# Performance work log

Measured on AMD Instinct MI355X. Metric: run time of the kernel, lower is better.

## Reference

```python
import jax, jax.numpy as jnp
import numpy as np

EPS_BN = 0.001

def setup_inputs() -> dict:
    key = jax.random.key(0)
    ks = jax.random.split(key, 11)
    B, C, H, W = 32, 512, 64, 64
    Hc = 128
    return {
        'x':  jax.random.normal(ks[0], (B, C, H, W), dtype=jnp.float32),
        'w1': jax.random.normal(ks[1], (Hc, C), dtype=jnp.float32) * (1.0 / np.sqrt(C)),
        'g1': jax.random.uniform(ks[2], (Hc,), dtype=jnp.float32, minval=0.5, maxval=1.5),
        'b1': jax.random.normal(ks[3], (Hc,), dtype=jnp.float32) * 0.1,
        'm1': jax.random.normal(ks[4], (Hc,), dtype=jnp.float32) * 0.1,
        'v1': jax.random.uniform(ks[5], (Hc,), dtype=jnp.float32, minval=0.5, maxval=1.5),
        'w2': jax.random.normal(ks[6], (C, Hc), dtype=jnp.float32) * (1.0 / np.sqrt(Hc)),
        'g2': jax.random.uniform(ks[7], (C,), dtype=jnp.float32, minval=0.5, maxval=1.5),
        'b2': jax.random.normal(ks[8], (C,), dtype=jnp.float32) * 0.1,
        'm2': jax.random.normal(ks[9], (C,), dtype=jnp.float32) * 0.1,
        'v2': jax.random.uniform(ks[10], (C,), dtype=jnp.float32, minval=0.5, maxval=1.5),
    }

def reference(x, w1, g1, b1, m1, v1, w2, g2, b2, m2, v2):
    # squeeze: global average pool -> [B, C]
    s = jnp.mean(x, axis=(2, 3))
    # excitation: 1x1 conv (C->Hc, no bias), eval-mode BN, ReLU, 1x1 conv (Hc->C, no bias)
    h = jnp.einsum('bc,hc->bh', s, w1)
    h = (h - m1) * (g1 * jax.lax.rsqrt(v1 + EPS_BN)) + b1
    h = jax.nn.relu(h)
    e = jnp.einsum('bh,ch->bc', h, w2)  # scale_activation = Identity
    # broadcast scale + final eval-mode BN over channels
    y = x * e[:, :, None, None]
    scale2 = (g2 * jax.lax.rsqrt(v2 + EPS_BN))[None, :, None, None]
    shift2 = (b2 - m2 * g2 * jax.lax.rsqrt(v2 + EPS_BN))[None, :, None, None]
    return y * scale2 + shift2
```

## Files before the change

### kernel.cpp

```cpp
#include <hip/hip_runtime.h>
#include <hip/hip_bf16.h>
#include <stdint.h>

#define B_   32
#define C_   512
#define HW_  4096
#define HC_  128
#define EPS_ 1e-3f

typedef uint32_t u32x4 __attribute__((ext_vector_type(4)));
typedef float    f32x4 __attribute__((ext_vector_type(4)));

__device__ __forceinline__ float bf_lo(uint32_t u) { return __uint_as_float(u << 16); }
__device__ __forceinline__ float bf_hi(uint32_t u) { return __uint_as_float(u & 0xffff0000u); }

__device__ __forceinline__ uint32_t packbf2(float lo, float hi) {
    union { uint32_t u; __hip_bfloat162 h; } cv;
    cv.h.x = __float2bfloat16(lo);
    cv.h.y = __float2bfloat16(hi);
    return cv.u;
}

__device__ __forceinline__ float ld_scalar(const void* p, int i, int isbf) {
    if (isbf) return __bfloat162float(((const __hip_bfloat16*)p)[i]);
    return ((const float*)p)[i];
}

template <int NT>
__device__ __forceinline__ int detect_isbf(const uint32_t* __restrict__ v2w,
                                           int t, int* s_flag) {
    if (t == 0) *s_flag = 1;
    __syncthreads();
    bool ok = true;
    #pragma unroll
    for (int i = t; i < 256; i += NT) {
        const uint32_t w = v2w[i];
        const float lo = bf_lo(w), hi = bf_hi(w);
        ok = ok && (lo >= 0.4f) && (lo <= 1.6f) && (hi >= 0.4f) && (hi <= 1.6f);
    }
    if (!ok) *s_flag = 0;
    __syncthreads();
    return *s_flag;
}

__global__ __launch_bounds__(256) void se_pool(const void* __restrict__ x,
                                               float* __restrict__ s,
                                               const uint32_t* __restrict__ v2w) {
    __shared__ int s_flag;
    __shared__ float part[4];
    const int t  = threadIdx.x;
    const int isbf = detect_isbf<256>(v2w, t, &s_flag);
    const int bc = blockIdx.x;
    float sum = 0.f;
    if (isbf) {
        const u32x4* p = reinterpret_cast<const u32x4*>(x) + (size_t)bc * (HW_ / 8);
        #pragma unroll
        for (int i = t; i < HW_ / 8; i += 256) {
            u32x4 v = p[i];
            sum += bf_lo(v.x) + bf_hi(v.x) + bf_lo(v.y) + bf_hi(v.y)
                 + bf_lo(v.z) + bf_hi(v.z) + bf_lo(v.w) + bf_hi(v.w);
        }
    } else {
        const f32x4* p = reinterpret_cast<const f32x4*>(x) + (size_t)bc * (HW_ / 4);
        #pragma unroll
        for (int i = t; i < HW_ / 4; i += 256) {
            f32x4 v = p[i];
            sum += v.x + v.y + v.z + v.w;
        }
    }
    #pragma unroll
    for (int off = 32; off > 0; off >>= 1)
        sum += __shfl_down(sum, off, 64);
    if ((t & 63) == 0) part[t >> 6] = sum;
    __syncthreads();
    if (t == 0) {
        float tot = part[0] + part[1] + part[2] + part[3];
        s[bc] = tot * (1.0f / (float)HW_);
    }
}

__global__ __launch_bounds__(128) void se_excite(
    const float* __restrict__ s,
    const void* __restrict__ w1, const void* __restrict__ g1,
    const void* __restrict__ b1, const void* __restrict__ m1,
    const void* __restrict__ v1, const void* __restrict__ w2,
    const void* __restrict__ g2, const void* __restrict__ b2,
    const void* __restrict__ m2, const void* __restrict__ v2,
    float* __restrict__ A, float* __restrict__ S2) {
    __shared__ int s_flag;
    __shared__ float s_sh[C_];
    __shared__ float h_sh[HC_];
    const int b = blockIdx.x, t = threadIdx.x;
    const int isbf = detect_isbf<128>((const uint32_t*)v2, t, &s_flag);
    for (int i = t; i < C_; i += HC_) s_sh[i] = s[b * C_ + i];
    __syncthreads();

    float acc = 0.f;
    if (isbf) {
        const u32x4* w1r = reinterpret_cast<const u32x4*>(w1) + (size_t)t * (C_ / 8);
        #pragma unroll 8
        for (int i = 0; i < C_ / 8; ++i) {
            u32x4 v = w1r[i];
            const int c = i * 8;
            acc += s_sh[c + 0] * bf_lo(v.x) + s_sh[c + 1] * bf_hi(v.x)
                 + s_sh[c + 2] * bf_lo(v.y) + s_sh[c + 3] * bf_hi(v.y)
                 + s_sh[c + 4] * bf_lo(v.z) + s_sh[c + 5] * bf_hi(v.z)
                 + s_sh[c + 6] * bf_lo(v.w) + s_sh[c + 7] * bf_hi(v.w);
        }
    } else {
        const f32x4* w1r = reinterpret_cast<const f32x4*>(w1) + (size_t)t * (C_ / 4);
        #pragma unroll 8
        for (int i = 0; i < C_ / 4; ++i) {
            f32x4 v = w1r[i];
            const int c = i * 4;
            acc += s_sh[c + 0] * v.x + s_sh[c + 1] * v.y
                 + s_sh[c + 2] * v.z + s_sh[c + 3] * v.w;
        }
    }
    const float sc1 = ld_scalar(g1, t, isbf) * rsqrtf(ld_scalar(v1, t, isbf) + EPS_);
    const float hv  = (acc - ld_scalar(m1, t, isbf)) * sc1 + ld_scalar(b1, t, isbf);
    h_sh[t] = fmaxf(hv, 0.f);
    __syncthreads();

    #pragma unroll
    for (int k = 0; k < C_ / HC_; ++k) {
        const int c = t + HC_ * k;
        float e = 0.f;
        if (isbf) {
            const u32x4* w2r = reinterpret_cast<const u32x4*>(w2) + (size_t)c * (HC_ / 8);
            #pragma unroll
            for (int i = 0; i < HC_ / 8; ++i) {
                u32x4 v = w2r[i];
                const int j = i * 8;
                e += h_sh[j + 0] * bf_lo(v.x) + h_sh[j + 1] * bf_hi(v.x)
                   + h_sh[j + 2] * bf_lo(v.y) + h_sh[j + 3] * bf_hi(v.y)
                   + h_sh[j + 4] * bf_lo(v.z) + h_sh[j + 5] * bf_hi(v.z)
                   + h_sh[j + 6] * bf_lo(v.w) + h_sh[j + 7] * bf_hi(v.w);
            }
        } else {
            const f32x4* w2r = reinterpret_cast<const f32x4*>(w2) + (size_t)c * (HC_ / 4);
            #pragma unroll
            for (int i = 0; i < HC_ / 4; ++i) {
                f32x4 v = w2r[i];
                const int j = i * 4;
                e += h_sh[j + 0] * v.x + h_sh[j + 1] * v.y
                   + h_sh[j + 2] * v.z + h_sh[j + 3] * v.w;
            }
        }
        const float sc2 = ld_scalar(g2, c, isbf) * rsqrtf(ld_scalar(v2, c, isbf) + EPS_);
        A[b * C_ + c] = e * sc2;
        if (b == 0) S2[c] = ld_scalar(b2, c, isbf) - ld_scalar(m2, c, isbf) * sc2;
    }
}

__global__ __launch_bounds__(256) void se_apply(const void* __restrict__ x,
                                                const float* __restrict__ A,
                                                const float* __restrict__ S2,
                                                void* __restrict__ y,
                                                const uint32_t* __restrict__ v2w) {
    __shared__ int s_flag;
    const int t  = threadIdx.x;
    const int isbf = detect_isbf<256>(v2w, t, &s_flag);
    const int bc = (B_ * C_ - 1) - (int)blockIdx.x;
    const float a  = A[bc];
    const float sh = S2[bc & (C_ - 1)];
    if (isbf) {
        const u32x4* px = reinterpret_cast<const u32x4*>(x) + (size_t)bc * (HW_ / 8);
        u32x4*       py = reinterpret_cast<u32x4*>(y)       + (size_t)bc * (HW_ / 8);
        #pragma unroll
        for (int i = t; i < HW_ / 8; i += 256) {
            u32x4 v = px[i];
            u32x4 r;
            r.x = packbf2(fmaf(bf_lo(v.x), a, sh), fmaf(bf_hi(v.x), a, sh));
            r.y = packbf2(fmaf(bf_lo(v.y), a, sh), fmaf(bf_hi(v.y), a, sh));
            r.z = packbf2(fmaf(bf_lo(v.z), a, sh), fmaf(bf_hi(v.z), a, sh));
            r.w = packbf2(fmaf(bf_lo(v.w), a, sh), fmaf(bf_hi(v.w), a, sh));
            __builtin_nontemporal_store(r, py + i);
        }
    } else {
        const f32x4* px = reinterpret_cast<const f32x4*>(x) + (size_t)bc * (HW_ / 4);
        f32x4*       py = reinterpret_cast<f32x4*>(y)       + (size_t)bc * (HW_ / 4);
        #pragma unroll
        for (int i = t; i < HW_ / 4; i += 256) {
            f32x4 v = px[i];
            f32x4 r;
            r.x = fmaf(v.x, a, sh);
            r.y = fmaf(v.y, a, sh);
            r.z = fmaf(v.z, a, sh);
            r.w = fmaf(v.w, a, sh);
            __builtin_nontemporal_store(r, py + i);
        }
    }
}

extern "C" void kernel_launch(void* const* d_in, const int* in_sizes, int n_in,
                              void* d_out, int out_size, void* d_ws, size_t ws_size,
                              hipStream_t stream) {
    const void* x  = d_in[0];
    const void* w1 = d_in[1];
    const void* g1 = d_in[2];
    const void* b1 = d_in[3];
    const void* m1 = d_in[4];
    const void* v1 = d_in[5];
    const void* w2 = d_in[6];
    const void* g2 = d_in[7];
    const void* b2 = d_in[8];
    const void* m2 = d_in[9];
    const void* v2 = d_in[10];

    float* ws = (float*)d_ws;
    float* s  = ws;
    float* A  = ws + B_ * C_;
    float* S2 = ws + 2 * B_ * C_;

    se_pool<<<B_ * C_, 256, 0, stream>>>(x, s, (const uint32_t*)v2);
    se_excite<<<B_, HC_, 0, stream>>>(s, w1, g1, b1, m1, v1, w2, g2, b2, m2, v2,
                                      A, S2);
    se_apply<<<B_ * C_, 256, 0, stream>>>(x, A, S2, d_out, (const uint32_t*)v2);
}
```

Measured before the change: 523.6 us.

## Fuse pooling and excitation via last-block-per-batch atomic counter

Merges the pooling and excitation kernels into one. Each block pools one (b,c) channel, then increments a per-batch atomic counter, and the last block to finish for a batch runs the two small matvecs. This drops one kernel launch and its serialization bubble, but adds a memset launch, threadfences and an atomic per block. The dtype-detection loop is also simplified to a single load per thread.

```diff
diff --git a/kernel.cpp b/kernel.cpp
--- a/kernel.cpp
+++ b/kernel.cpp
@@ -26,108 +26,110 @@
     return ((const float*)p)[i];
 }
 
-template <int NT>
 __device__ __forceinline__ int detect_isbf(const uint32_t* __restrict__ v2w,
                                            int t, int* s_flag) {
     if (t == 0) *s_flag = 1;
     __syncthreads();
-    bool ok = true;
-    #pragma unroll
-    for (int i = t; i < 256; i += NT) {
-        const uint32_t w = v2w[i];
-        const float lo = bf_lo(w), hi = bf_hi(w);
-        ok = ok && (lo >= 0.4f) && (lo <= 1.6f) && (hi >= 0.4f) && (hi <= 1.6f);
-    }
+    const uint32_t w = v2w[t];
+    const float lo = bf_lo(w), hi = bf_hi(w);
+    const bool ok = (lo >= 0.4f) && (lo <= 1.6f) && (hi >= 0.4f) && (hi <= 1.6f);
     if (!ok) *s_flag = 0;
     __syncthreads();
     return *s_flag;
 }
 
-__global__ __launch_bounds__(256) void se_pool(const void* __restrict__ x,
-                                               float* __restrict__ s,
-                                               const uint32_t* __restrict__ v2w) {
-    __shared__ int s_flag;
-    __shared__ float part[4];
-    const int t  = threadIdx.x;
-    const int isbf = detect_isbf<256>(v2w, t, &s_flag);
-    const int bc = blockIdx.x;
-    float sum = 0.f;
-    if (isbf) {
-        const u32x4* p = reinterpret_cast<const u32x4*>(x) + (size_t)bc * (HW_ / 8);
-        #pragma unroll
-        for (int i = t; i < HW_ / 8; i += 256) {
-            u32x4 v = p[i];
-            sum += bf_lo(v.x) + bf_hi(v.x) + bf_lo(v.y) + bf_hi(v.y)
-                 + bf_lo(v.z) + bf_hi(v.z) + bf_lo(v.w) + bf_hi(v.w);
-        }
-    } else {
-        const f32x4* p = reinterpret_cast<const f32x4*>(x) + (size_t)bc * (HW_ / 4);
-        #pragma unroll
-        for (int i = t; i < HW_ / 4; i += 256) {
-            f32x4 v = p[i];
-            sum += v.x + v.y + v.z + v.w;
-        }
-    }
-    #pragma unroll
-    for (int off = 32; off > 0; off >>= 1)
-        sum += __shfl_down(sum, off, 64);
-    if ((t & 63) == 0) part[t >> 6] = sum;
-    __syncthreads();
-    if (t == 0) {
-        float tot = part[0] + part[1] + part[2] + part[3];
-        s[bc] = tot * (1.0f / (float)HW_);
-    }
-}
-
-__global__ __launch_bounds__(128) void se_excite(
-    const float* __restrict__ s,
+__global__ __launch_bounds__(256) void se_pool_excite(
+    const void* __restrict__ x,
     const void* __restrict__ w1, const void* __restrict__ g1,
     const void* __restrict__ b1, const void* __restrict__ m1,
     const void* __restrict__ v1, const void* __restrict__ w2,
     const void* __restrict__ g2, const void* __restrict__ b2,
     const void* __restrict__ m2, const void* __restrict__ v2,
-    float* __restrict__ A, float* __restrict__ S2) {
-    __shared__ int s_flag;
+    float* __restrict__ s, float* __restrict__ A, float* __restrict__ S2,
+    int* __restrict__ cnt)
+{
+    __shared__ int   s_flag;
+    __shared__ int   s_last;
+    __shared__ float part[4];
     __shared__ float s_sh[C_];
     __shared__ float h_sh[HC_];
-    const int b = blockIdx.x, t = threadIdx.x;
-    const int isbf = detect_isbf<128>((const uint32_t*)v2, t, &s_flag);
-    for (int i = t; i < C_; i += HC_) s_sh[i] = s[b * C_ + i];
-    __syncthreads();
-
-    float acc = 0.f;
+
+    const int t    = threadIdx.x;
+    const int bc   = blockIdx.x;
+    const int b    = bc >> 9;
+    const int isbf = detect_isbf((const uint32_t*)v2, t, &s_flag);
+
+    float sum = 0.f;
     if (isbf) {
-        const u32x4* w1r = reinterpret_cast<const u32x4*>(w1) + (size_t)t * (C_ / 8);
-        #pragma unroll 8
-        for (int i = 0; i < C_ / 8; ++i) {
-            u32x4 v = w1r[i];
-            const int c = i * 8;
-            acc += s_sh[c + 0] * bf_lo(v.x) + s_sh[c + 1] * bf_hi(v.x)
-                 + s_sh[c + 2] * bf_lo(v.y) + s_sh[c + 3] * bf_hi(v.y)
-                 + s_sh[c + 4] * bf_lo(v.z) + s_sh[c + 5] * bf_hi(v.z)
-                 + s_sh[c + 6] * bf_lo(v.w) + s_sh[c + 7] * bf_hi(v.w);
+        const u32x4* p = (const u32x4*)x + (size_t)bc * (HW_ / 8);
+        #pragma unroll
+        for (int i = t; i < HW_ / 8; i += 256) {
+            u32x4 v = p[i];
+            sum += bf_lo(v.x) + bf_hi(v.x) + bf_lo(v.y) + bf_hi(v.y)
+                 + bf_lo(v.z) + bf_hi(v.z) + bf_lo(v.w) + bf_hi(v.w);
         }
     } else {
-        const f32x4* w1r = reinterpret_cast<const f32x4*>(w1) + (size_t)t * (C_ / 4);
-        #pragma unroll 8
-        for (int i = 0; i < C_ / 4; ++i) {
-            f32x4 v = w1r[i];
-            const int c = i * 4;
-            acc += s_sh[c + 0] * v.x + s_sh[c + 1] * v.y
-                 + s_sh[c + 2] * v.z + s_sh[c + 3] * v.w;
-        }
-    }
-    const float sc1 = ld_scalar(g1, t, isbf) * rsqrtf(ld_scalar(v1, t, isbf) + EPS_);
-    const float hv  = (acc - ld_scalar(m1, t, isbf)) * sc1 + ld_scalar(b1, t, isbf);
-    h_sh[t] = fmaxf(hv, 0.f);
-    __syncthreads();
-
+        const f32x4* p = (const f32x4*)x + (size_t)bc * (HW_ / 4);
+        #pragma unroll
+        for (int i = t; i < HW_ / 4; i += 256) {
+            f32x4 v = p[i];
+            sum += v.x + v.y + v.z + v.w;
+        }
+    }
     #pragma unroll
-    for (int k = 0; k < C_ / HC_; ++k) {
-        const int c = t + HC_ * k;
+    for (int off = 32; off > 0; off >>= 1)
+        sum += __shfl_down(sum, off, 64);
+    if ((t & 63) == 0) part[t >> 6] = sum;
+    __syncthreads();
+    if (t == 0) {
+        const float tot = part[0] + part[1] + part[2] + part[3];
+        s[bc] = tot * (1.0f / (float)HW_);
+        __threadfence();
+        const int old = atomicAdd(&cnt[b], 1);
+        s_last = (old == C_ - 1) ? 1 : 0;
+    }
+    __syncthreads();
+    if (!s_last) return;
+
+    __threadfence();
+    for (int i = t; i < C_; i += 256) s_sh[i] = s[b * C_ + i];
+    __syncthreads();
+
+    if (t < HC_) {
+        float acc = 0.f;
+        if (isbf) {
+            const u32x4* w1r = (const u32x4*)w1 + (size_t)t * (C_ / 8);
+            #pragma unroll 8
+            for (int i = 0; i < C_ / 8; ++i) {
+                u32x4 v = w1r[i];
+                const int c = i * 8;
+                acc += s_sh[c + 0] * bf_lo(v.x) + s_sh[c + 1] * bf_hi(v.x)
+                     + s_sh[c + 2] * bf_lo(v.y) + s_sh[c + 3] * bf_hi(v.y)
+                     + s_sh[c + 4] * bf_lo(v.z) + s_sh[c + 5] * bf_hi(v.z)
+                     + s_sh[c + 6] * bf_lo(v.w) + s_sh[c + 7] * bf_hi(v.w);
+            }
+        } else {
+            const f32x4* w1r = (const f32x4*)w1 + (size_t)t * (C_ / 4);
+            #pragma unroll 8
+            for (int i = 0; i < C_ / 4; ++i) {
+                f32x4 v = w1r[i];
+                const int c = i * 4;
+                acc += s_sh[c + 0] * v.x + s_sh[c + 1] * v.y
+                     + s_sh[c + 2] * v.z + s_sh[c + 3] * v.w;
+            }
+        }
+        const float sc1 = ld_scalar(g1, t, isbf) * rsqrtf(ld_scalar(v1, t, isbf) + EPS_);
+        const float hv  = (acc - ld_scalar(m1, t, isbf)) * sc1 + ld_scalar(b1, t, isbf);
+        h_sh[t] = fmaxf(hv, 0.f);
+    }
+    __syncthreads();
+
+    #pragma unroll
+    for (int k = 0; k < 2; ++k) {
+        const int c = t + 256 * k;
         float e = 0.f;
         if (isbf) {
-            const u32x4* w2r = reinterpret_cast<const u32x4*>(w2) + (size_t)c * (HC_ / 8);
+            const u32x4* w2r = (const u32x4*)w2 + (size_t)c * (HC_ / 8);
             #pragma unroll
             for (int i = 0; i < HC_ / 8; ++i) {
                 u32x4 v = w2r[i];
@@ -138,7 +140,7 @@
                    + h_sh[j + 6] * bf_lo(v.w) + h_sh[j + 7] * bf_hi(v.w);
             }
         } else {
-            const f32x4* w2r = reinterpret_cast<const f32x4*>(w2) + (size_t)c * (HC_ / 4);
+            const f32x4* w2r = (const f32x4*)w2 + (size_t)c * (HC_ / 4);
             #pragma unroll
             for (int i = 0; i < HC_ / 4; ++i) {
                 f32x4 v = w2r[i];
@@ -160,13 +162,13 @@
                                                 const uint32_t* __restrict__ v2w) {
     __shared__ int s_flag;
     const int t  = threadIdx.x;
-    const int isbf = detect_isbf<256>(v2w, t, &s_flag);
+    const int isbf = detect_isbf(v2w, t, &s_flag);
     const int bc = (B_ * C_ - 1) - (int)blockIdx.x;
     const float a  = A[bc];
     const float sh = S2[bc & (C_ - 1)];
     if (isbf) {
-        const u32x4* px = reinterpret_cast<const u32x4*>(x) + (size_t)bc * (HW_ / 8);
-        u32x4*       py = reinterpret_cast<u32x4*>(y)       + (size_t)bc * (HW_ / 8);
+        const u32x4* px = (const u32x4*)x + (size_t)bc * (HW_ / 8);
+        u32x4*       py = (u32x4*)y       + (size_t)bc * (HW_ / 8);
         #pragma unroll
         for (int i = t; i < HW_ / 8; i += 256) {
             u32x4 v = px[i];
@@ -178,8 +180,8 @@
             __builtin_nontemporal_store(r, py + i);
         }
     } else {
-        const f32x4* px = reinterpret_cast<const f32x4*>(x) + (size_t)bc * (HW_ / 4);
-        f32x4*       py = reinterpret_cast<f32x4*>(y)       + (size_t)bc * (HW_ / 4);
+        const f32x4* px = (const f32x4*)x + (size_t)bc * (HW_ / 4);
+        f32x4*       py = (f32x4*)y       + (size_t)bc * (HW_ / 4);
         #pragma unroll
         for (int i = t; i < HW_ / 4; i += 256) {
             f32x4 v = px[i];
@@ -212,9 +214,12 @@
     float* s  = ws;
     float* A  = ws + B_ * C_;
     float* S2 = ws + 2 * B_ * C_;
-
-    se_pool<<<B_ * C_, 256, 0, stream>>>(x, s, (const uint32_t*)v2);
-    se_excite<<<B_, HC_, 0, stream>>>(s, w1, g1, b1, m1, v1, w2, g2, b2, m2, v2,
-                                      A, S2);
+    int*  cnt = (int*)(ws + 2 * B_ * C_ + C_);
+
+    hipMemsetAsync(cnt, 0, B_ * sizeof(int), stream);
+
+    se_pool_excite<<<B_ * C_, 256, 0, stream>>>(x, w1, g1, b1, m1, v1,
+                                                w2, g2, b2, m2, v2,
+                                                s, A, S2, cnt);
     se_apply<<<B_ * C_, 256, 0, stream>>>(x, A, S2, d_out, (const uint32_t*)v2);
 }
```

New measurement: 1.212 ms. 2.31x slower.
